# Performance work log

Measured on AMD Instinct MI355X. Metric: run time of the kernel, lower is better.

The kernel has to match this reference:

```python
import jax, jax.numpy as jnp
import numpy as np

N = 50000
E = 800000
IN_DIM, HID, OUT_DIM = 768, 256, 128
BN_EPS = 1e-5
NORM_EPS = 1e-12


def setup_inputs() -> dict:
    key = jax.random.key(0)
    ks = jax.random.split(key, 16)
    inp = {
        "x": jax.random.normal(ks[0], (N, IN_DIM), dtype=jnp.float32),
        "edge_index": jax.random.randint(ks[1], (2, E), 0, N, dtype=jnp.int64),
        "edge_weight": jax.random.uniform(ks[2], (E,), dtype=jnp.float32),
        # GCNConv weights (PyG: out = scatter(norm * (x @ W)[src]) + b)
        "W1": jax.random.normal(ks[3], (IN_DIM, HID), dtype=jnp.float32) * 0.02,
        "b1": jnp.zeros((HID,), jnp.float32),
        "W2": jax.random.normal(ks[4], (HID, HID), dtype=jnp.float32) * 0.02,
        "b2": jnp.zeros((HID,), jnp.float32),
        "W3": jax.random.normal(ks[5], (HID, OUT_DIM), dtype=jnp.float32) * 0.02,
        "b3": jnp.zeros((OUT_DIM,), jnp.float32),
        # BatchNorm (eval mode: running stats)
        "bn1_gamma": jnp.ones((HID,), jnp.float32),
        "bn1_beta": jnp.zeros((HID,), jnp.float32),
        "bn1_mean": jax.random.normal(ks[6], (HID,), dtype=jnp.float32) * 0.1,
        "bn1_var": jax.random.uniform(ks[7], (HID,), dtype=jnp.float32) + 0.5,
        "bn2_gamma": jnp.ones((HID,), jnp.float32),
        "bn2_beta": jnp.zeros((HID,), jnp.float32),
        "bn2_mean": jax.random.normal(ks[8], (HID,), dtype=jnp.float32) * 0.1,
        "bn2_var": jax.random.uniform(ks[9], (HID,), dtype=jnp.float32) + 0.5,
    }
    return inp


def _gcn_norm(edge_index, edge_weight, n):
    # add self loops with weight 1 (PyG GCNConv default)
    src = jnp.concatenate([edge_index[0], jnp.arange(n, dtype=edge_index.dtype)])
    dst = jnp.concatenate([edge_index[1], jnp.arange(n, dtype=edge_index.dtype)])
    ew = jnp.concatenate([edge_weight, jnp.ones((n,), edge_weight.dtype)])
    deg = jax.ops.segment_sum(ew, dst, num_segments=n)  # [N]
    dis = jnp.where(deg > 0, jax.lax.rsqrt(deg), 0.0)
    norm = dis[src] * ew * dis[dst]  # [E+N]
    return src, dst, norm


def _gcn_conv(h, W, b, src, dst, norm, n):
    h = h @ W                                  # [N, F_out]
    msg = h[src] * norm[:, None]               # gather + scale, [E+N, F_out]
    out = jax.ops.segment_sum(msg, dst, num_segments=n)  # scatter-add
    return out + b


def _bn_eval(h, gamma, beta, mean, var):
    return (h - mean) * jax.lax.rsqrt(var + BN_EPS) * gamma + beta


def reference(x, edge_index, edge_weight,
              W1, b1, W2, b2, W3, b3,
              bn1_gamma, bn1_beta, bn1_mean, bn1_var,
              bn2_gamma, bn2_beta, bn2_mean, bn2_var):
    n = x.shape[0]
    src, dst, norm = _gcn_norm(edge_index, edge_weight, n)
    h = _gcn_conv(x, W1, b1, src, dst, norm, n)
    h = jax.nn.relu(_bn_eval(h, bn1_gamma, bn1_beta, bn1_mean, bn1_var))
    h = _gcn_conv(h, W2, b2, src, dst, norm, n)
    h = jax.nn.relu(_bn_eval(h, bn2_gamma, bn2_beta, bn2_mean, bn2_var))
    h = _gcn_conv(h, W3, b3, src, dst, norm, n)
    # F.normalize(x, p=2, dim=1): x / max(||x||, eps)
    nrm = jnp.sqrt(jnp.sum(h * h, axis=1, keepdims=True))
    return h / jnp.maximum(nrm, NORM_EPS)
```

## Files before the change

### kernel.cpp

```cpp
#include <hip/hip_runtime.h>
#include <cstddef>

#define NN 50000
#define EE 800000
#define NB 196

typedef __attribute__((ext_vector_type(8))) _Float16 f16x8;
typedef __attribute__((ext_vector_type(4))) _Float16 f16x4;
typedef __attribute__((ext_vector_type(2))) _Float16 f16x2;
typedef __attribute__((ext_vector_type(4))) float f32x4;

__device__ __forceinline__ unsigned pk2h(float a, float b) {
  auto h = __builtin_amdgcn_cvt_pkrtz(a, b);
  return __builtin_bit_cast(unsigned, h);
}

__global__ void k_zero_off(int* __restrict__ off) {
  int i = blockIdx.x * 256 + threadIdx.x;
  if (i <= NN) off[i] = 0;
}

__global__ void k_count(const int* __restrict__ src, const int* __restrict__ dst,
                        int* __restrict__ off) {
  int e = blockIdx.x * 256 + threadIdx.x;
  if (e < EE) {
    int s = src[e], d = dst[e];
    if (s >= 0 && s < NN && d >= 0 && d < NN) atomicAdd(&off[d], 1);
  }
}

__global__ void k_scanA(int* __restrict__ off, int* __restrict__ bsum) {
  __shared__ int sh[256];
  int t = threadIdx.x;
  int idx = blockIdx.x * 256 + t;
  int v = (idx < NN) ? off[idx] : 0;
  sh[t] = v;
  __syncthreads();
  for (int d = 1; d < 256; d <<= 1) {
    int x = (t >= d) ? sh[t - d] : 0;
    __syncthreads();
    sh[t] += x;
    __syncthreads();
  }
  if (idx < NN) off[idx] = sh[t] - v;
  if (t == 255) bsum[blockIdx.x] = sh[255];
}

__global__ void k_scanB(int* __restrict__ bsum, int* __restrict__ bpre,
                        int* __restrict__ off) {
  __shared__ int sh[256];
  int t = threadIdx.x;
  int v = (t < NB) ? bsum[t] : 0;
  sh[t] = v;
  __syncthreads();
  for (int d = 1; d < 256; d <<= 1) {
    int x = (t >= d) ? sh[t - d] : 0;
    __syncthreads();
    sh[t] += x;
    __syncthreads();
  }
  if (t < NB) bpre[t] = sh[t] - v;
  if (t == 255) off[NN] = sh[255];
}

__global__ void k_scanC(int* __restrict__ off, const int* __restrict__ bpre,
                        int* __restrict__ cursor) {
  int idx = blockIdx.x * 256 + threadIdx.x;
  if (idx < NN) {
    int o = off[idx] + bpre[blockIdx.x];
    off[idx] = o;
    cursor[idx] = o;
  }
}

__global__ void k_fill(const int* __restrict__ src, const int* __restrict__ dst,
                       const float* __restrict__ ew, int* __restrict__ cursor,
                       int* __restrict__ csrc, float* __restrict__ cew) {
  int e = blockIdx.x * 256 + threadIdx.x;
  if (e < EE) {
    int s = src[e], d = dst[e];
    if (s >= 0 && s < NN && d >= 0 && d < NN) {
      int p = atomicAdd(&cursor[d], 1);
      csrc[p] = s;
      cew[p] = ew[e];
    }
  }
}

__global__ void k_degdis(const int* __restrict__ off, const float* __restrict__ cew,
                         float* __restrict__ dis) {
  int i = blockIdx.x * 256 + threadIdx.x;
  if (i >= NN) return;
  int e0 = off[i], e1 = off[i + 1];
  float s = 1.0f;
  for (int e = e0; e < e1; ++e) s += cew[e];
  dis[i] = rsqrtf(s);
}

__global__ void k_affine(const float* __restrict__ g1, const float* __restrict__ be1,
                         const float* __restrict__ m1, const float* __restrict__ v1,
                         const float* __restrict__ g2, const float* __restrict__ be2,
                         const float* __restrict__ m2, const float* __restrict__ v2,
                         float* __restrict__ s1, float* __restrict__ u1,
                         float* __restrict__ s2, float* __restrict__ u2) {
  int f = threadIdx.x;
  float a1 = g1[f] * rsqrtf(v1[f] + 1e-5f);
  s1[f] = a1; u1[f] = be1[f] - m1[f] * a1;
  float a2 = g2[f] * rsqrtf(v2[f] + 1e-5f);
  s2[f] = a2; u2[f] = be2[f] - m2[f] * a2;
}

__global__ void k_wt(const float* __restrict__ W, _Float16* __restrict__ WT,
                     int K, int N) {
  int k = blockIdx.x * 256 + threadIdx.x;
  int n = blockIdx.y;
  if (k < K) WT[(size_t)n * K + k] = (_Float16)W[(size_t)k * N + n];
}

#define LDA 40
__global__ __launch_bounds__(256) void k_gemm_mfma(const void* __restrict__ Ain,
                                                   const _Float16* __restrict__ BT,
                                                   _Float16* __restrict__ C,
                                                   int M, int K, int Nout, int a_fp32) {
  __shared__ _Float16 As[128 * LDA];
  __shared__ _Float16 Bs[128 * LDA];
  const int tid = threadIdx.x;
  const int bm = blockIdx.y << 7;
  const int bn = blockIdx.x << 7;
  const int lane = tid & 63;
  const int wid = tid >> 6;
  const int wm = (wid & 1) << 6;
  const int wn = (wid >> 1) << 6;
  const int quad = lane >> 4;
  const int l16 = lane & 15;

  f32x4 acc[4][4] = {};

  for (int k0 = 0; k0 < K; k0 += 32) {
#pragma unroll
    for (int j = 0; j < 2; ++j) {
      int c = tid + (j << 8);
      int row = c >> 2, kc = c & 3;
      uint4 va = make_uint4(0, 0, 0, 0);
      int gr = bm + row;
      if (gr < M) {
        if (a_fp32) {
          const float* p = (const float*)Ain + (size_t)gr * K + k0 + (kc << 3);
          float4 f0 = *(const float4*)p;
          float4 f1 = *(const float4*)(p + 4);
          va.x = pk2h(f0.x, f0.y);
          va.y = pk2h(f0.z, f0.w);
          va.z = pk2h(f1.x, f1.y);
          va.w = pk2h(f1.z, f1.w);
        } else {
          va = *(const uint4*)((const _Float16*)Ain + (size_t)gr * K + k0 + (kc << 3));
        }
      }
      *(uint4*)&As[row * LDA + (kc << 3)] = va;
      uint4 vb = *(const uint4*)(BT + (size_t)(bn + row) * K + k0 + (kc << 3));
      *(uint4*)&Bs[row * LDA + (kc << 3)] = vb;
    }
    __syncthreads();
    f16x8 af[4], bfr[4];
#pragma unroll
    for (int mt = 0; mt < 4; ++mt)
      af[mt] = *(const f16x8*)&As[(wm + (mt << 4) + l16) * LDA + (quad << 3)];
#pragma unroll
    for (int nt = 0; nt < 4; ++nt)
      bfr[nt] = *(const f16x8*)&Bs[(wn + (nt << 4) + l16) * LDA + (quad << 3)];
#pragma unroll
    for (int mt = 0; mt < 4; ++mt)
#pragma unroll
      for (int nt = 0; nt < 4; ++nt)
        acc[mt][nt] = __builtin_amdgcn_mfma_f32_16x16x32_f16(af[mt], bfr[nt], acc[mt][nt], 0, 0, 0);
    __syncthreads();
  }

  const int rbase = bm + wm + (quad << 2);
#pragma unroll
  for (int mt = 0; mt < 4; ++mt) {
#pragma unroll
    for (int reg = 0; reg < 4; ++reg) {
      int r = rbase + (mt << 4) + reg;
      if (r < M) {
        _Float16* crow = C + (size_t)r * Nout + bn + wn + l16;
#pragma unroll
        for (int nt = 0; nt < 4; ++nt) crow[nt << 4] = (_Float16)acc[mt][nt][reg];
      }
    }
  }
}

__global__ __launch_bounds__(256) void k_agg256(const _Float16* __restrict__ hW,
                                                const float* __restrict__ dis,
                                                const float* __restrict__ b,
                                                const int* __restrict__ off,
                                                const int* __restrict__ csrc,
                                                const float* __restrict__ cew,
                                                const float* __restrict__ s,
                                                const float* __restrict__ u,
                                                _Float16* __restrict__ hout) {
  int i = (blockIdx.x << 2) + (threadIdx.x >> 6);
  if (i >= NN) return;
  int lane = threadIdx.x & 63;
  float di = dis[i];
  float4 bb = *(const float4*)(b + (lane << 2));
  f16x4 hv = *(const f16x4*)(hW + (size_t)i * 256 + (lane << 2));
  float d2 = di * di;
  float4 acc;
  acc.x = fmaf((float)hv.x, d2, bb.x);
  acc.y = fmaf((float)hv.y, d2, bb.y);
  acc.z = fmaf((float)hv.z, d2, bb.z);
  acc.w = fmaf((float)hv.w, d2, bb.w);
  int e0 = off[i], e1 = off[i + 1];
  int e = e0;
  for (; e + 3 < e1; e += 4) {
    int sa = csrc[e], sb = csrc[e + 1], sc = csrc[e + 2], sd = csrc[e + 3];
    float wa = dis[sa] * cew[e] * di;
    float wb = dis[sb] * cew[e + 1] * di;
    float wc = dis[sc] * cew[e + 2] * di;
    float wd = dis[sd] * cew[e + 3] * di;
    f16x4 ra = *(const f16x4*)(hW + (size_t)sa * 256 + (lane << 2));
    f16x4 rb = *(const f16x4*)(hW + (size_t)sb * 256 + (lane << 2));
    f16x4 rc = *(const f16x4*)(hW + (size_t)sc * 256 + (lane << 2));
    f16x4 rd = *(const f16x4*)(hW + (size_t)sd * 256 + (lane << 2));
    acc.x = fmaf((float)ra.x, wa, acc.x); acc.y = fmaf((float)ra.y, wa, acc.y);
    acc.z = fmaf((float)ra.z, wa, acc.z); acc.w = fmaf((float)ra.w, wa, acc.w);
    acc.x = fmaf((float)rb.x, wb, acc.x); acc.y = fmaf((float)rb.y, wb, acc.y);
    acc.z = fmaf((float)rb.z, wb, acc.z); acc.w = fmaf((float)rb.w, wb, acc.w);
    acc.x = fmaf((float)rc.x, wc, acc.x); acc.y = fmaf((float)rc.y, wc, acc.y);
    acc.z = fmaf((float)rc.z, wc, acc.z); acc.w = fmaf((float)rc.w, wc, acc.w);
    acc.x = fmaf((float)rd.x, wd, acc.x); acc.y = fmaf((float)rd.y, wd, acc.y);
    acc.z = fmaf((float)rd.z, wd, acc.z); acc.w = fmaf((float)rd.w, wd, acc.w);
  }
  for (; e < e1; ++e) {
    int sa = csrc[e];
    float wa = dis[sa] * cew[e] * di;
    f16x4 ra = *(const f16x4*)(hW + (size_t)sa * 256 + (lane << 2));
    acc.x = fmaf((float)ra.x, wa, acc.x); acc.y = fmaf((float)ra.y, wa, acc.y);
    acc.z = fmaf((float)ra.z, wa, acc.z); acc.w = fmaf((float)ra.w, wa, acc.w);
  }
  float4 sv = *(const float4*)(s + (lane << 2));
  float4 uv = *(const float4*)(u + (lane << 2));
  float r0 = fmaxf(fmaf(acc.x, sv.x, uv.x), 0.f);
  float r1 = fmaxf(fmaf(acc.y, sv.y, uv.y), 0.f);
  float r2 = fmaxf(fmaf(acc.z, sv.z, uv.z), 0.f);
  float r3 = fmaxf(fmaf(acc.w, sv.w, uv.w), 0.f);
  uint2 pk;
  pk.x = pk2h(r0, r1);
  pk.y = pk2h(r2, r3);
  *(uint2*)&hout[(size_t)i * 256 + (lane << 2)] = pk;
}

__global__ __launch_bounds__(256) void k_agg128_l2(const _Float16* __restrict__ hW,
                                                   const float* __restrict__ dis,
                                                   const float* __restrict__ b,
                                                   const int* __restrict__ off,
                                                   const int* __restrict__ csrc,
                                                   const float* __restrict__ cew,
                                                   float* __restrict__ out) {
  int i = (blockIdx.x << 2) + (threadIdx.x >> 6);
  if (i >= NN) return;
  int lane = threadIdx.x & 63;
  float di = dis[i];
  float2 bb = *(const float2*)(b + (lane << 1));
  f16x2 hv = *(const f16x2*)(hW + (size_t)i * 128 + (lane << 1));
  float d2 = di * di;
  float2 acc;
  acc.x = fmaf((float)hv.x, d2, bb.x);
  acc.y = fmaf((float)hv.y, d2, bb.y);
  int e0 = off[i], e1 = off[i + 1];
  int e = e0;
  for (; e + 3 < e1; e += 4) {
    int sa = csrc[e], sb = csrc[e + 1], sc = csrc[e + 2], sd = csrc[e + 3];
    float wa = dis[sa] * cew[e] * di;
    float wb = dis[sb] * cew[e + 1] * di;
    float wc = dis[sc] * cew[e + 2] * di;
    float wd = dis[sd] * cew[e + 3] * di;
    f16x2 ra = *(const f16x2*)(hW + (size_t)sa * 128 + (lane << 1));
    f16x2 rb = *(const f16x2*)(hW + (size_t)sb * 128 + (lane << 1));
    f16x2 rc = *(const f16x2*)(hW + (size_t)sc * 128 + (lane << 1));
    f16x2 rd = *(const f16x2*)(hW + (size_t)sd * 128 + (lane << 1));
    acc.x = fmaf((float)ra.x, wa, acc.x); acc.y = fmaf((float)ra.y, wa, acc.y);
    acc.x = fmaf((float)rb.x, wb, acc.x); acc.y = fmaf((float)rb.y, wb, acc.y);
    acc.x = fmaf((float)rc.x, wc, acc.x); acc.y = fmaf((float)rc.y, wc, acc.y);
    acc.x = fmaf((float)rd.x, wd, acc.x); acc.y = fmaf((float)rd.y, wd, acc.y);
  }
  for (; e < e1; ++e) {
    int sa = csrc[e];
    float wa = dis[sa] * cew[e] * di;
    f16x2 ra = *(const f16x2*)(hW + (size_t)sa * 128 + (lane << 1));
    acc.x = fmaf((float)ra.x, wa, acc.x); acc.y = fmaf((float)ra.y, wa, acc.y);
  }
  float ss = fmaf(acc.x, acc.x, acc.y * acc.y);
#pragma unroll
  for (int o = 32; o > 0; o >>= 1) ss += __shfl_xor(ss, o, 64);
  float sc2 = 1.0f / fmaxf(sqrtf(ss), 1e-12f);
  acc.x *= sc2;
  acc.y *= sc2;
  *(float2*)(out + (size_t)i * 128 + (lane << 1)) = acc;
}

extern "C" void kernel_launch(void* const* d_in, const int* in_sizes, int n_in,
                              void* d_out, int out_size, void* d_ws, size_t ws_size,
                              hipStream_t stream) {
  const size_t OFF_CUR = 50176, OFF_BS = 100352, OFF_BP = 100608;
  const size_t OFF_CS = 100864, OFF_CW = 900864, OFF_DIS = 1700864;
  const size_t OFF_AFF = 1751040, OFF_HW = 1752064;
  const size_t OFF_HB = OFF_HW + (size_t)NN * 256;
  const size_t OFF_WT1 = OFF_HB + (size_t)NN * 128;
  const size_t OFF_WT2 = OFF_WT1 + 768 * 256 / 2;
  const size_t OFF_WT3 = OFF_WT2 + 256 * 256 / 2;
  const size_t WS_UNITS = OFF_WT3 + 256 * 128 / 2 + 256;
  if (ws_size < WS_UNITS * 4) return;

  const float* x  = (const float*)d_in[0];
  const int* ei   = (const int*)d_in[1];
  const float* ew = (const float*)d_in[2];
  const float* W1 = (const float*)d_in[3];
  const float* b1 = (const float*)d_in[4];
  const float* W2 = (const float*)d_in[5];
  const float* b2 = (const float*)d_in[6];
  const float* W3 = (const float*)d_in[7];
  const float* b3 = (const float*)d_in[8];
  const float* g1 = (const float*)d_in[9];
  const float* be1 = (const float*)d_in[10];
  const float* m1 = (const float*)d_in[11];
  const float* v1 = (const float*)d_in[12];
  const float* g2 = (const float*)d_in[13];
  const float* be2 = (const float*)d_in[14];
  const float* m2 = (const float*)d_in[15];
  const float* v2 = (const float*)d_in[16];
  float* out = (float*)d_out;
  const int* src = ei;
  const int* dstp = ei + EE;

  int* wsi = (int*)d_ws;
  float* wsf = (float*)d_ws;
  int* off = wsi;
  int* cursor = wsi + OFF_CUR;
  int* bsum = wsi + OFF_BS;
  int* bpre = wsi + OFF_BP;
  int* csrc = wsi + OFF_CS;
  float* cew = wsf + OFF_CW;
  float* dis = wsf + OFF_DIS;
  float* s1 = wsf + OFF_AFF;
  float* u1 = s1 + 256;
  float* s2 = u1 + 256;
  float* u2 = s2 + 256;
  _Float16* hW = (_Float16*)(wsf + OFF_HW);
  _Float16* hb = (_Float16*)(wsi + OFF_HB);
  _Float16* wT1 = (_Float16*)(wsi + OFF_WT1);
  _Float16* wT2 = (_Float16*)(wsi + OFF_WT2);
  _Float16* wT3 = (_Float16*)(wsi + OFF_WT3);

  dim3 b256(256);
  const int EB = (EE + 255) / 256;
  k_zero_off<<<NB, b256, 0, stream>>>(off);
  k_count<<<EB, b256, 0, stream>>>(src, dstp, off);
  k_scanA<<<NB, b256, 0, stream>>>(off, bsum);
  k_scanB<<<1, b256, 0, stream>>>(bsum, bpre, off);
  k_scanC<<<NB, b256, 0, stream>>>(off, bpre, cursor);
  k_fill<<<EB, b256, 0, stream>>>(src, dstp, ew, cursor, csrc, cew);
  k_degdis<<<NB, b256, 0, stream>>>(off, cew, dis);
  k_affine<<<1, b256, 0, stream>>>(g1, be1, m1, v1, g2, be2, m2, v2, s1, u1, s2, u2);
  k_wt<<<dim3(3, 256), b256, 0, stream>>>(W1, wT1, 768, 256);
  k_wt<<<dim3(1, 256), b256, 0, stream>>>(W2, wT2, 256, 256);
  k_wt<<<dim3(1, 128), b256, 0, stream>>>(W3, wT3, 256, 128);

  const int GM = (NN + 127) / 128;
  const int AGB = (NN + 3) / 4;
  k_gemm_mfma<<<dim3(2, GM), b256, 0, stream>>>(x, wT1, hW, NN, 768, 256, 1);
  k_agg256<<<AGB, b256, 0, stream>>>(hW, dis, b1, off, csrc, cew, s1, u1, hb);
  k_gemm_mfma<<<dim3(2, GM), b256, 0, stream>>>(hb, wT2, hW, NN, 256, 256, 0);
  k_agg256<<<AGB, b256, 0, stream>>>(hW, dis, b2, off, csrc, cew, s2, u2, hb);
  k_gemm_mfma<<<dim3(1, GM), b256, 0, stream>>>(hb, wT3, hW, NN, 256, 128, 0);
  k_agg128_l2<<<AGB, b256, 0, stream>>>(hW, dis, b3, off, csrc, cew, out);
}
```

Baseline: 633.2 us.

## Replace LDS-tiled GEMM with register-resident A rows and streamed B fragments

The shared-memory tiled MFMA GEMM is replaced by a templated kernel in which each wave keeps its 16 rows of A for the full K dimension in registers and computes every output column. B fragments are loaded straight from global memory (expected to stay cached, since the weights are small) through a software-pipelined register ring of configurable depth. This removes LDS staging and barriers and reads A only once, instead of once per N-tile. In exchange it uses far more registers (up to 24 f16x8 A fragments plus 16 accumulators for layer 1), which limits occupancy, and every wave re-reads B from cache.

```diff
diff --git a/kernel.cpp b/kernel.cpp
--- a/kernel.cpp
+++ b/kernel.cpp
@@ -117,76 +117,80 @@
   if (k < K) WT[(size_t)n * K + k] = (_Float16)W[(size_t)k * N + n];
 }
 
-#define LDA 40
-__global__ __launch_bounds__(256) void k_gemm_mfma(const void* __restrict__ Ain,
-                                                   const _Float16* __restrict__ BT,
-                                                   _Float16* __restrict__ C,
-                                                   int M, int K, int Nout, int a_fp32) {
-  __shared__ _Float16 As[128 * LDA];
-  __shared__ _Float16 Bs[128 * LDA];
+template <int A32, int K, int NOUT, int MINW, int DEPTH>
+__global__ __launch_bounds__(256, MINW) void k_gemm(const void* __restrict__ Ain,
+                                                    const _Float16* __restrict__ BT,
+                                                    _Float16* __restrict__ C,
+                                                    int M) {
+  constexpr int T = K / 32;
+  constexpr int NG = NOUT / 64;
+  constexpr int G = T * NG;
+  constexpr int NC = NOUT / 16;
+
   const int tid = threadIdx.x;
-  const int bm = blockIdx.y << 7;
-  const int bn = blockIdx.x << 7;
   const int lane = tid & 63;
   const int wid = tid >> 6;
-  const int wm = (wid & 1) << 6;
-  const int wn = (wid >> 1) << 6;
   const int quad = lane >> 4;
   const int l16 = lane & 15;
-
-  f32x4 acc[4][4] = {};
-
-  for (int k0 = 0; k0 < K; k0 += 32) {
-#pragma unroll
-    for (int j = 0; j < 2; ++j) {
-      int c = tid + (j << 8);
-      int row = c >> 2, kc = c & 3;
-      uint4 va = make_uint4(0, 0, 0, 0);
-      int gr = bm + row;
-      if (gr < M) {
-        if (a_fp32) {
-          const float* p = (const float*)Ain + (size_t)gr * K + k0 + (kc << 3);
-          float4 f0 = *(const float4*)p;
-          float4 f1 = *(const float4*)(p + 4);
-          va.x = pk2h(f0.x, f0.y);
-          va.y = pk2h(f0.z, f0.w);
-          va.z = pk2h(f1.x, f1.y);
-          va.w = pk2h(f1.z, f1.w);
-        } else {
-          va = *(const uint4*)((const _Float16*)Ain + (size_t)gr * K + k0 + (kc << 3));
-        }
-      }
-      *(uint4*)&As[row * LDA + (kc << 3)] = va;
-      uint4 vb = *(const uint4*)(BT + (size_t)(bn + row) * K + k0 + (kc << 3));
-      *(uint4*)&Bs[row * LDA + (kc << 3)] = vb;
+  const int wrow = blockIdx.x * 64 + wid * 16;
+  const int arow = wrow + l16;
+  const int arc = (arow < M) ? arow : 0;
+
+  f16x8 aK[T];
+  if (A32) {
+    const float* ap = (const float*)Ain + (size_t)arc * K + (quad << 3);
+#pragma unroll
+    for (int t = 0; t < T; ++t) {
+      float4 u = *(const float4*)(ap + t * 32);
+      float4 v = *(const float4*)(ap + t * 32 + 4);
+      aK[t] = __builtin_bit_cast(f16x8,
+          make_uint4(pk2h(u.x, u.y), pk2h(u.z, u.w), pk2h(v.x, v.y), pk2h(v.z, v.w)));
     }
-    __syncthreads();
-    f16x8 af[4], bfr[4];
-#pragma unroll
-    for (int mt = 0; mt < 4; ++mt)
-      af[mt] = *(const f16x8*)&As[(wm + (mt << 4) + l16) * LDA + (quad << 3)];
-#pragma unroll
-    for (int nt = 0; nt < 4; ++nt)
-      bfr[nt] = *(const f16x8*)&Bs[(wn + (nt << 4) + l16) * LDA + (quad << 3)];
-#pragma unroll
-    for (int mt = 0; mt < 4; ++mt)
-#pragma unroll
-      for (int nt = 0; nt < 4; ++nt)
-        acc[mt][nt] = __builtin_amdgcn_mfma_f32_16x16x32_f16(af[mt], bfr[nt], acc[mt][nt], 0, 0, 0);
-    __syncthreads();
-  }
-
-  const int rbase = bm + wm + (quad << 2);
-#pragma unroll
-  for (int mt = 0; mt < 4; ++mt) {
-#pragma unroll
-    for (int reg = 0; reg < 4; ++reg) {
-      int r = rbase + (mt << 4) + reg;
-      if (r < M) {
-        _Float16* crow = C + (size_t)r * Nout + bn + wn + l16;
-#pragma unroll
-        for (int nt = 0; nt < 4; ++nt) crow[nt << 4] = (_Float16)acc[mt][nt][reg];
-      }
+  } else {
+    const _Float16* ap = (const _Float16*)Ain + (size_t)arc * K + (quad << 3);
+#pragma unroll
+    for (int t = 0; t < T; ++t) aK[t] = *(const f16x8*)(ap + t * 32);
+  }
+
+  const _Float16* bbase = BT + (size_t)l16 * K + (quad << 3);
+  f32x4 acc[NC];
+#pragma unroll
+  for (int c = 0; c < NC; ++c) acc[c] = (f32x4){0.f, 0.f, 0.f, 0.f};
+  f16x8 bs[DEPTH][4];
+
+#define LOADB(g)                                                              \
+  do {                                                                        \
+    int t_ = (g) / NG, p_ = (g) % NG;                                         \
+    _Pragma("unroll") for (int j = 0; j < 4; ++j)                             \
+        bs[(g) % DEPTH][j] =                                                  \
+            *(const f16x8*)(bbase + (size_t)((p_ * 4 + j) * 16) * K + t_ * 32); \
+  } while (0)
+
+#define DOMF(g)                                                               \
+  do {                                                                        \
+    int t_ = (g) / NG, p_ = (g) % NG;                                         \
+    _Pragma("unroll") for (int j = 0; j < 4; ++j)                             \
+        acc[p_ * 4 + j] = __builtin_amdgcn_mfma_f32_16x16x32_f16(             \
+            aK[t_], bs[(g) % DEPTH][j], acc[p_ * 4 + j], 0, 0, 0);            \
+  } while (0)
+
+#pragma unroll
+  for (int g = 0; g < DEPTH - 1 && g < G; ++g) LOADB(g);
+#pragma unroll
+  for (int g = 0; g < G; ++g) {
+    if (g + DEPTH - 1 < G) LOADB(g + DEPTH - 1);
+    DOMF(g);
+  }
+#undef LOADB
+#undef DOMF
+
+  const int rb = wrow + (quad << 2);
+#pragma unroll
+  for (int c = 0; c < NC; ++c) {
+#pragma unroll
+    for (int r = 0; r < 4; ++r) {
+      int row = rb + r;
+      if (row < M) C[(size_t)row * NOUT + c * 16 + l16] = (_Float16)acc[c][r];
     }
   }
 }
@@ -368,12 +372,12 @@
   k_wt<<<dim3(1, 256), b256, 0, stream>>>(W2, wT2, 256, 256);
   k_wt<<<dim3(1, 128), b256, 0, stream>>>(W3, wT3, 256, 128);
 
-  const int GM = (NN + 127) / 128;
+  const int GB = (NN + 63) / 64;
   const int AGB = (NN + 3) / 4;
-  k_gemm_mfma<<<dim3(2, GM), b256, 0, stream>>>(x, wT1, hW, NN, 768, 256, 1);
+  k_gemm<1, 768, 256, 2, 2><<<GB, b256, 0, stream>>>(x, wT1, hW, NN);
   k_agg256<<<AGB, b256, 0, stream>>>(hW, dis, b1, off, csrc, cew, s1, u1, hb);
-  k_gemm_mfma<<<dim3(2, GM), b256, 0, stream>>>(hb, wT2, hW, NN, 256, 256, 0);
+  k_gemm<0, 256, 256, 2, 3><<<GB, b256, 0, stream>>>(hb, wT2, hW, NN);
   k_agg256<<<AGB, b256, 0, stream>>>(hW, dis, b2, off, csrc, cew, s2, u2, hb);
-  k_gemm_mfma<<<dim3(1, GM), b256, 0, stream>>>(hb, wT3, hW, NN, 256, 128, 0);
+  k_gemm<0, 256, 128, 3, 3><<<GB, b256, 0, stream>>>(hb, wT3, hW, NN);
   k_agg128_l2<<<AGB, b256, 0, stream>>>(hW, dis, b3, off, csrc, cew, out);
 }
```

New measurement: 793.4 us. 1.25x slower.
